# Performance work log

Hardware: AMD Instinct MI355X
Metric: run time of the kernel (lower is better)

The kernel has to match this reference:

```python
import jax, jax.numpy as jnp
import numpy as np


def setup_inputs() -> dict:
    key = jax.random.key(0)
    ks = jax.random.split(key, 8)
    B, L, D, H, Dh = 2, 2048, 1024, 16, 64
    scale = 1.0 / np.sqrt(D)
    return {
        "inputs_q": jax.random.normal(ks[0], (B, L, D), jnp.float32),
        "inputs_kv": jax.random.normal(ks[1], (B, L, D), jnp.float32),
        "mask_k": jax.random.uniform(ks[2], (B, L), jnp.float32),
        "Wq": jax.random.normal(ks[3], (D, H, Dh), jnp.float32) * scale,
        "bq": jnp.zeros((H, Dh), jnp.float32),
        "Wk": jax.random.normal(ks[4], (D, H, Dh), jnp.float32) * scale,
        "bk": jnp.zeros((H, Dh), jnp.float32),
        "Wv": jax.random.normal(ks[5], (D, H, Dh), jnp.float32) * scale,
        "bv": jnp.zeros((H, Dh), jnp.float32),
        "Wo": jax.random.normal(ks[6], (H, Dh, D), jnp.float32) * (1.0 / np.sqrt(D)),
        "bo": jnp.zeros((D,), jnp.float32),
    }


def reference(inputs_q, inputs_kv, mask_k, Wq, bq, Wk, bk, Wv, bv, Wo, bo):
    # QKV projections: [B,L,D] x [D,H,Dh] -> [B,L,H,Dh]
    q = jnp.einsum("bld,dhk->blhk", inputs_q, Wq) + bq
    k = jnp.einsum("bld,dhk->blhk", inputs_kv, Wk) + bk
    v = jnp.einsum("bld,dhk->blhk", inputs_kv, Wv) + bv
    # vector mask applied to values per key position
    v = mask_k[:, :, None, None] * v
    head_dim = q.shape[-1]
    q = q / jnp.sqrt(jnp.asarray(head_dim, q.dtype))
    # attention scores [B,H,Lq,Lk]
    scores = jnp.einsum("bqhk,bshk->bhqs", q, k)
    probs = jax.nn.softmax(scores, axis=-1)
    # weighted values [B,Lq,H,Dh]
    x = jnp.einsum("bhqs,bshk->bqhk", probs, v)
    # output projection over (head, head_dim)
    out = jnp.einsum("bqhk,hkd->bqd", x, Wo) + bo
    return out
```

## Files before the change

### kernel.cpp

```cpp
#include <hip/hip_runtime.h>
#include <stdint.h>

typedef __attribute__((ext_vector_type(8))) short bf16x8;
typedef __attribute__((ext_vector_type(4))) float f32x4;
typedef __attribute__((ext_vector_type(16))) float f32x16;
typedef __attribute__((ext_vector_type(4))) unsigned short us4;
typedef __attribute__((ext_vector_type(4))) unsigned int u32x4;

#define AS1 __attribute__((address_space(1)))
#define AS3 __attribute__((address_space(3)))

static constexpr int Lq = 2048;
static constexpr int Dm = 1024;
static constexpr int NH = 16;
static constexpr int DH = 64;

__device__ __forceinline__ unsigned short f2bf(float x) {
  union { float f; uint32_t u; } v; v.f = x;
  uint32_t r = v.u + 0x7FFFu + ((v.u >> 16) & 1u);
  return (unsigned short)(r >> 16);
}

#if __has_builtin(__builtin_amdgcn_exp2f)
__device__ __forceinline__ float exp2_fast(float x) { return __builtin_amdgcn_exp2f(x); }
#else
__device__ __forceinline__ float exp2_fast(float x) {
  float r; asm volatile("v_exp_f32 %0, %1" : "=v"(r) : "v"(x)); return r;
}
#endif

__device__ __forceinline__ uint32_t cvtpk_bf16(float lo, float hi) {
  uint32_t r;
  asm("v_cvt_pk_bf16_f32 %0, %1, %2" : "=v"(r) : "v"(lo), "v"(hi));
  return r;
}

__device__ __forceinline__ f32x16 zero16() {
  f32x16 z;
#pragma unroll
  for (int i = 0; i < 16; ++i) z[i] = 0.f;
  return z;
}

__global__ __launch_bounds__(256) void cvt2_kernel(
    const float* __restrict__ s0, const float* __restrict__ s1,
    unsigned short* __restrict__ d0, unsigned short* __restrict__ d1, int n4) {
  const float* src = blockIdx.y ? s1 : s0;
  unsigned short* dst = blockIdx.y ? d1 : d0;
  int idx = blockIdx.x * 256 + threadIdx.x;
  int stride = gridDim.x * 256;
  for (int i = idx; i < n4; i += stride) {
    float4 f = ((const float4*)src)[i];
    us4 o = { f2bf(f.x), f2bf(f.y), f2bf(f.z), f2bf(f.w) };
    ((us4*)dst)[i] = o;
  }
}

__global__ __launch_bounds__(256) void tpose_kernel(
    const float* __restrict__ W0, const float* __restrict__ W1,
    const float* __restrict__ W2, const float* __restrict__ W3,
    unsigned short* __restrict__ T0, unsigned short* __restrict__ T1,
    unsigned short* __restrict__ T2, unsigned short* __restrict__ T3) {
  __shared__ float tile[32][33];
  const float* src; unsigned short* dst;
  switch (blockIdx.z) {
    case 0: src = W0; dst = T0; break;
    case 1: src = W1; dst = T1; break;
    case 2: src = W2; dst = T2; break;
    default: src = W3; dst = T3; break;
  }
  int x = threadIdx.x & 31, ys = threadIdx.x >> 5;
  int bx = blockIdx.x * 32, by = blockIdx.y * 32;
  for (int i = 0; i < 4; ++i) {
    int y = ys * 4 + i;
    tile[y][x] = src[(size_t)(by + y) * Dm + bx + x];
  }
  __syncthreads();
  for (int i = 0; i < 4; ++i) {
    int y = ys * 4 + i;
    dst[(size_t)(bx + y) * Dm + by + x] = f2bf(tile[x][y]);
  }
}

__global__ __launch_bounds__(256) void gemm_kernel(
    const unsigned short* __restrict__ A0, const unsigned short* __restrict__ A1,
    const unsigned short* __restrict__ W0, const unsigned short* __restrict__ W1,
    const unsigned short* __restrict__ W2,
    const float* __restrict__ b0, const float* __restrict__ b1,
    const float* __restrict__ b2, const float* __restrict__ mask,
    unsigned short* __restrict__ Qw, unsigned short* __restrict__ Kw,
    unsigned short* __restrict__ Vtw, float* __restrict__ Of, int modeBase) {
  const int mode = modeBase + blockIdx.z;
  const unsigned short* Ap = (mode == 1 || mode == 2) ? A1 : A0;
  const unsigned short* Wp = (mode == 1) ? W1 : ((mode == 2) ? W2 : W0);
  const float* bias = (mode == 1) ? b1 : ((mode == 2) ? b2 : b0);

  const int tid = threadIdx.x, lane = tid & 63, wid = tid >> 6;
  const int wm = wid >> 1, wn = wid & 1;
  const int m0 = blockIdx.x * 128, n0 = blockIdx.y * 128;
  const int ln = lane & 15, kg = lane >> 4;

  __shared__ __align__(16) unsigned short smem[24576];

  f32x4 acc[4][4];
#pragma unroll
  for (int i = 0; i < 4; ++i)
#pragma unroll
    for (int j = 0; j < 4; ++j) acc[i][j] = f32x4{0.f, 0.f, 0.f, 0.f};

  auto stage_g = [&](int buf, int k0) {
#pragma unroll
    for (int i = 0; i < 2; ++i) {
      const int t = i * 256 + tid;
      const int row = t >> 2, ch = t & 3;
      const int tb = i * 256 + wid * 64;
      __builtin_amdgcn_global_load_lds(
          (const AS1 unsigned int*)(Ap + (size_t)(m0 + row) * Dm + k0 + ch * 8),
          (AS3 unsigned int*)&smem[buf * 4096 + tb * 8], 16, 0, 0);
      __builtin_amdgcn_global_load_lds(
          (const AS1 unsigned int*)(Wp + (size_t)(n0 + row) * Dm + k0 + ch * 8),
          (AS3 unsigned int*)&smem[12288 + buf * 4096 + tb * 8], 16, 0, 0);
    }
  };
  auto comp_g = [&](int buf) {
    const unsigned short* As = &smem[buf * 4096];
    const unsigned short* Bs = &smem[12288 + buf * 4096];
    bf16x8 af[4], bfv[4];
#pragma unroll
    for (int f = 0; f < 4; ++f) {
      af[f]  = *(const bf16x8*)&As[(wm * 64 + f * 16 + ln) * 32 + kg * 8];
      bfv[f] = *(const bf16x8*)&Bs[(wn * 64 + f * 16 + ln) * 32 + kg * 8];
    }
    __builtin_amdgcn_s_setprio(1);
#pragma unroll
    for (int mf = 0; mf < 4; ++mf)
#pragma unroll
      for (int nf = 0; nf < 4; ++nf)
        acc[mf][nf] = __builtin_amdgcn_mfma_f32_16x16x32_bf16(af[mf], bfv[nf],
                                                              acc[mf][nf], 0, 0, 0);
    __builtin_amdgcn_s_setprio(0);
  };

  stage_g(0, 0);
  stage_g(1, 32);
  for (int tt = 0; tt < 30; tt += 3) {
#pragma unroll
    for (int j = 0; j < 3; ++j) {
      const int t = tt + j;
      asm volatile("s_waitcnt vmcnt(4)" ::: "memory");
      asm volatile("s_barrier" ::: "memory");
      if (t < 30) stage_g((j + 2) % 3, (t + 2) * 32);
      comp_g(j);
    }
  }
  asm volatile("s_waitcnt vmcnt(4)" ::: "memory");
  asm volatile("s_barrier" ::: "memory");
  comp_g(0);
  asm volatile("s_waitcnt vmcnt(0)" ::: "memory");
  asm volatile("s_barrier" ::: "memory");
  comp_g(1);

  __syncthreads();
  unsigned short* ep = smem + wid * 2304;
  const int rowbase = m0 + wm * 64;
  const int colbase = n0 + wn * 64;

  if (mode <= 1) {
    unsigned short* dstbase = (mode == 0) ? Qw : Kw;
    const int hh = colbase >> 6;
    const int bb_ = rowbase >> 11, lb = rowbase & 2047;
    unsigned short* dst = dstbase + ((size_t)(bb_ * NH + hh) * Lq + lb) * DH;
    const float sc = (mode == 0) ? 0.18033688f : 1.0f;
    for (int p = 0; p < 2; ++p) {
      for (int nf = 0; nf < 4; ++nf) {
        const float bv_ = bias[colbase + nf * 16 + ln];
        for (int mh = 0; mh < 2; ++mh) {
          const int mf = 2 * p + mh;
          const int rl2 = mh * 16 + kg * 4;
          for (int r = 0; r < 4; ++r)
            ep[(rl2 + r) * 72 + nf * 16 + ln] = f2bf((acc[mf][nf][r] + bv_) * sc);
        }
      }
      for (int it = 0; it < 4; ++it) {
        const int e = it * 64 + lane;
        const int rr = e >> 3, c = (e & 7) * 8;
        *(bf16x8*)(dst + (size_t)(p * 32 + rr) * DH + c) = *(const bf16x8*)&ep[rr * 72 + c];
      }
    }
  } else if (mode == 2) {
    const int hh = colbase >> 6;
    const int bb_ = rowbase >> 11;
    const int l0 = rowbase & 2047;
    unsigned short* dst = Vtw + (size_t)(bb_ * NH + hh) * DH * Lq;
    for (int p = 0; p < 2; ++p) {
      for (int nh2 = 0; nh2 < 2; ++nh2) {
        const int nf = 2 * p + nh2;
        const int dh2 = nh2 * 16 + ln;
        const float bv_ = bias[colbase + nf * 16 + ln];
        for (int mf = 0; mf < 4; ++mf)
          for (int r = 0; r < 4; ++r) {
            const int rl = mf * 16 + kg * 4 + r;
            ep[dh2 * 72 + rl] = f2bf((acc[mf][nf][r] + bv_) * mask[rowbase + rl]);
          }
      }
      for (int it = 0; it < 4; ++it) {
        const int e = it * 64 + lane;
        const int dr = e >> 3, c = (e & 7) * 8;
        *(bf16x8*)(dst + (size_t)(p * 32 + dr) * Lq + l0 + c) = *(const bf16x8*)&ep[dr * 72 + c];
      }
    }
  } else {
    float* epf = (float*)smem + wid * 1152;
    for (int mf = 0; mf < 4; ++mf) {
      for (int nf = 0; nf < 4; ++nf) {
        const float bv_ = bias[colbase + nf * 16 + ln];
        for (int r = 0; r < 4; ++r)
          epf[(kg * 4 + r) * 68 + nf * 16 + ln] = acc[mf][nf][r] + bv_;
      }
      for (int it = 0; it < 4; ++it) {
        const int e = it * 64 + lane;
        const int rr = e >> 4, c = (lane & 15) * 4;
        *(f32x4*)(Of + (size_t)(rowbase + mf * 16 + rr) * Dm + colbase + c) =
            *(const f32x4*)&epf[rr * 68 + c];
      }
    }
  }
}

__global__ __launch_bounds__(512) void attn_kernel(
    const unsigned short* __restrict__ Q, const unsigned short* __restrict__ K,
    const unsigned short* __restrict__ Vt, unsigned short* __restrict__ X) {
  const int tid = threadIdx.x, lane = tid & 63, wv = tid >> 6;
  const int lq = lane & 31, hi = lane >> 5;
  const int wq = wv & 3, half = wv >> 2;
  const int h = blockIdx.y, b = blockIdx.z;
  const int q0 = blockIdx.x * 128 + wq * 32;

  const size_t bh = (size_t)b * NH + h;
  const unsigned short* Qp = Q + bh * Lq * DH;
  const unsigned short* Kp = K + bh * Lq * DH + (size_t)half * 1024 * DH;
  const unsigned short* Vp = Vt + bh * DH * Lq + half * 1024;

  __shared__ __align__(16) unsigned short smem[24576];
  unsigned short* Klds = smem + half * 12288;
  unsigned short* Vlds = smem + half * 12288 + 6144;

  const int st = tid & 255;
  const int kr = st >> 3, kc = st & 7;
  const unsigned short* ksrc = Kp + (size_t)kr * DH + ((kc ^ (kr & 7)) * 8);
  const int vr = st >> 2, vc = st & 3;
  const unsigned short* vsrc = Vp + (size_t)vr * Lq + ((vc ^ ((vr >> 1) & 3)) * 8);

  auto stage = [&](int buf, const unsigned short* kp, const unsigned short* vp) {
    __builtin_amdgcn_global_load_lds((const AS1 unsigned int*)kp,
        (AS3 unsigned int*)&Klds[buf * 2048 + wq * 512], 16, 0, 0);
    __builtin_amdgcn_global_load_lds((const AS1 unsigned int*)vp,
        (AS3 unsigned int*)&Vlds[buf * 2048 + wq * 512], 16, 0, 0);
  };

  bf16x8 qf[4];
#pragma unroll
  for (int ks = 0; ks < 4; ++ks)
    qf[ks] = *(const bf16x8*)(Qp + (size_t)(q0 + lq) * DH + ks * 16 + hi * 8);

  f32x16 o0 = zero16(), o1 = zero16();
  float lsum = 0.f;

  auto compute = [&](const unsigned short* Kb, const unsigned short* Vb) {
    f32x16 s0 = zero16(), s1 = zero16();
    __builtin_amdgcn_s_setprio(1);
#pragma unroll
    for (int ks = 0; ks < 4; ++ks) {
      const bf16x8 kfr =
          *(const bf16x8*)&Kb[lq * 64 + (((2 * ks + hi) ^ (lq & 7)) * 8)];
      if (ks < 2) s0 = __builtin_amdgcn_mfma_f32_32x32x16_bf16(kfr, qf[ks], s0, 0, 0, 0);
      else        s1 = __builtin_amdgcn_mfma_f32_32x32x16_bf16(kfr, qf[ks], s1, 0, 0, 0);
    }
    __builtin_amdgcn_s_setprio(0);

    float p[16];
#pragma unroll
    for (int i = 0; i < 16; ++i) p[i] = exp2_fast(s0[i] + s1[i]);
    lsum += ((((p[0] + p[1]) + (p[2] + p[3])) + ((p[4] + p[5]) + (p[6] + p[7]))) +
             (((p[8] + p[9]) + (p[10] + p[11])) + ((p[12] + p[13]) + (p[14] + p[15]))));

    uint32_t a00 = cvtpk_bf16(p[0],  p[1]),  a01 = cvtpk_bf16(p[2],  p[3]);
    uint32_t a10 = cvtpk_bf16(p[4],  p[5]),  a11 = cvtpk_bf16(p[6],  p[7]);
    uint32_t a20 = cvtpk_bf16(p[8],  p[9]),  a21 = cvtpk_bf16(p[10], p[11]);
    uint32_t a30 = cvtpk_bf16(p[12], p[13]), a31 = cvtpk_bf16(p[14], p[15]);
    asm volatile("v_permlane32_swap_b32 %0, %1" : "+v"(a00), "+v"(a10));
    asm volatile("v_permlane32_swap_b32 %0, %1" : "+v"(a01), "+v"(a11));
    asm volatile("v_permlane32_swap_b32 %0, %1" : "+v"(a20), "+v"(a30));
    asm volatile("v_permlane32_swap_b32 %0, %1" : "+v"(a21), "+v"(a31));
    u32x4 pw0 = {a00, a01, a10, a11};
    u32x4 pw1 = {a20, a21, a30, a31};
    const bf16x8 pa0 = *(const bf16x8*)&pw0;
    const bf16x8 pa1 = *(const bf16x8*)&pw1;

    __builtin_amdgcn_s_setprio(1);
    {
      const int sw0 = (lq >> 1) & 3;
      const bf16x8 vb0 = *(const bf16x8*)&Vb[lq * 32 + ((hi ^ sw0) * 8)];
      const bf16x8 vb1 = *(const bf16x8*)&Vb[lq * 32 + (((2 + hi) ^ sw0) * 8)];
      o0 = __builtin_amdgcn_mfma_f32_32x32x16_bf16(pa0, vb0, o0, 0, 0, 0);
      o0 = __builtin_amdgcn_mfma_f32_32x32x16_bf16(pa1, vb1, o0, 0, 0, 0);
      const int dh1 = 32 + lq;
      const int sw1 = (dh1 >> 1) & 3;
      const bf16x8 vb2 = *(const bf16x8*)&Vb[dh1 * 32 + ((hi ^ sw1) * 8)];
      const bf16x8 vb3 = *(const bf16x8*)&Vb[dh1 * 32 + (((2 + hi) ^ sw1) * 8)];
      o1 = __builtin_amdgcn_mfma_f32_32x32x16_bf16(pa0, vb2, o1, 0, 0, 0);
      o1 = __builtin_amdgcn_mfma_f32_32x32x16_bf16(pa1, vb3, o1, 0, 0, 0);
    }
    __builtin_amdgcn_s_setprio(0);
  };

  stage(0, ksrc, vsrc);
  stage(1, ksrc + 2048, vsrc + 32);
  const unsigned short* kpre = ksrc + 4096;
  const unsigned short* vpre = vsrc + 64;
  for (int tt = 0; tt < 30; tt += 3) {
#pragma unroll
    for (int j = 0; j < 3; ++j) {
      asm volatile("s_waitcnt vmcnt(2)" ::: "memory");
      asm volatile("s_barrier" ::: "memory");
      stage((j + 2) % 3, kpre, vpre);
      kpre += 2048; vpre += 32;
      compute(&Klds[j * 2048], &Vlds[j * 2048]);
    }
  }
  asm volatile("s_waitcnt vmcnt(2)" ::: "memory");
  asm volatile("s_barrier" ::: "memory");
  compute(&Klds[0], &Vlds[0]);
  asm volatile("s_waitcnt vmcnt(0)" ::: "memory");
  asm volatile("s_barrier" ::: "memory");
  compute(&Klds[2048], &Vlds[2048]);

  lsum += __shfl_xor(lsum, 32);
  __syncthreads();
  float* cs = (float*)smem;
  float* po = cs + wq * 2048;
  float* pl = cs + 8192 + wq * 32;
  if (half == 1) {
#pragma unroll
    for (int r = 0; r < 16; ++r) {
      const int qrow = (r & 3) + 8 * (r >> 2) + 4 * hi;
      po[qrow * 64 + lq]      = o0[r];
      po[qrow * 64 + 32 + lq] = o1[r];
    }
    if (hi == 0) pl[lq] = lsum;
  }
  __syncthreads();
  if (half == 0) {
#pragma unroll
    for (int r = 0; r < 16; ++r) {
      const int qrow = (r & 3) + 8 * (r >> 2) + 4 * hi;
      o0[r] += po[qrow * 64 + lq];
      o1[r] += po[qrow * 64 + 32 + lq];
    }
    lsum += pl[lq];
    const float inv = 1.0f / lsum;
    unsigned short* ep = (unsigned short*)po;
#pragma unroll
    for (int r = 0; r < 16; ++r) {
      const int qrow = (r & 3) + 8 * (r >> 2) + 4 * hi;
      const float iv = __shfl(inv, qrow);
      ep[qrow * 72 + lq]      = f2bf(o0[r] * iv);
      ep[qrow * 72 + 32 + lq] = f2bf(o1[r] * iv);
    }
#pragma unroll
    for (int it = 0; it < 4; ++it) {
      const int e = it * 64 + lane;
      const int row = e >> 3, ch = e & 7;
      *(bf16x8*)(X + (size_t)(b * Lq + q0 + row) * Dm + h * DH + ch * 8) =
          *(const bf16x8*)&ep[row * 72 + ch * 8];
    }
  }
}

extern "C" void kernel_launch(void* const* d_in, const int* in_sizes, int n_in,
                              void* d_out, int out_size, void* d_ws, size_t ws_size,
                              hipStream_t stream) {
  (void)in_sizes; (void)n_in; (void)out_size; (void)ws_size;
  const float* inputs_q  = (const float*)d_in[0];
  const float* inputs_kv = (const float*)d_in[1];
  const float* mask_k    = (const float*)d_in[2];
  const float* Wq = (const float*)d_in[3];
  const float* bq = (const float*)d_in[4];
  const float* Wk = (const float*)d_in[5];
  const float* bk = (const float*)d_in[6];
  const float* Wv = (const float*)d_in[7];
  const float* bv = (const float*)d_in[8];
  const float* Wo = (const float*)d_in[9];
  const float* bo = (const float*)d_in[10];
  float* out = (float*)d_out;

  unsigned short* ws = (unsigned short*)d_ws;
  const size_t BIG = 4194304;
  const size_t WSZ = 1048576;
  unsigned short* Xq  = ws;
  unsigned short* Xkv = Xq + BIG;
  unsigned short* Wqt = Xkv + BIG;
  unsigned short* Wkt = Wqt + WSZ;
  unsigned short* Wvt = Wkt + WSZ;
  unsigned short* Wot = Wvt + WSZ;
  unsigned short* Qw  = Wot + WSZ;
  unsigned short* Kw  = Qw + BIG;
  unsigned short* Vtw = Kw + BIG;
  unsigned short* Xat = Vtw + BIG;

  cvt2_kernel<<<dim3(512, 2), 256, 0, stream>>>(inputs_q, inputs_kv, Xq, Xkv,
                                                (int)(BIG / 4));
  tpose_kernel<<<dim3(32, 32, 4), 256, 0, stream>>>(Wq, Wk, Wv, Wo, Wqt, Wkt, Wvt, Wot);
  gemm_kernel<<<dim3(32, 8, 3), 256, 0, stream>>>(Xq, Xkv, Wqt, Wkt, Wvt, bq, bk, bv,
                                                  mask_k, Qw, Kw, Vtw, nullptr, 0);
  attn_kernel<<<dim3(16, 16, 2), 512, 0, stream>>>(Qw, Kw, Vtw, Xat);
  gemm_kernel<<<dim3(32, 8, 1), 256, 0, stream>>>(Xat, nullptr, Wot, nullptr, nullptr,
                                                  bo, nullptr, nullptr, nullptr,
                                                  nullptr, nullptr, nullptr, out, 3);
}
```

Before: 117.3 us.

## Use 8-wave GEMM blocks with swizzled LDS, MFMA row-sum in attention

The GEMM kernel now runs 512 threads per 128x128 tile, so each wave computes a 32x64 sub-tile, and LDS staging uses an XOR swizzle to cut bank conflicts on fragment reads. In attention, the two score accumulators are merged into one, and the softmax row sum is computed by an extra MFMA against a ones vector instead of scalar adds and a shuffle. The final normalisation is also restructured. This trades fewer accumulator registers per wave and more waves for less scalar work, at the cost of extra MFMA issue and bf16-rounded probabilities feeding the row sum.

```diff
diff --git a/kernel.cpp b/kernel.cpp
--- a/kernel.cpp
+++ b/kernel.cpp
@@ -82,7 +82,7 @@
   }
 }
 
-__global__ __launch_bounds__(256) void gemm_kernel(
+__global__ __launch_bounds__(512) void gemm_kernel(
     const unsigned short* __restrict__ A0, const unsigned short* __restrict__ A1,
     const unsigned short* __restrict__ W0, const unsigned short* __restrict__ W1,
     const unsigned short* __restrict__ W2,
@@ -102,38 +102,36 @@
 
   __shared__ __align__(16) unsigned short smem[24576];
 
-  f32x4 acc[4][4];
-#pragma unroll
-  for (int i = 0; i < 4; ++i)
+  f32x4 acc[2][4];
+#pragma unroll
+  for (int i = 0; i < 2; ++i)
 #pragma unroll
     for (int j = 0; j < 4; ++j) acc[i][j] = f32x4{0.f, 0.f, 0.f, 0.f};
 
+  const int srow = tid >> 2;
+  const int schx = (tid & 3) ^ ((srow >> 1) & 3);
   auto stage_g = [&](int buf, int k0) {
-#pragma unroll
-    for (int i = 0; i < 2; ++i) {
-      const int t = i * 256 + tid;
-      const int row = t >> 2, ch = t & 3;
-      const int tb = i * 256 + wid * 64;
-      __builtin_amdgcn_global_load_lds(
-          (const AS1 unsigned int*)(Ap + (size_t)(m0 + row) * Dm + k0 + ch * 8),
-          (AS3 unsigned int*)&smem[buf * 4096 + tb * 8], 16, 0, 0);
-      __builtin_amdgcn_global_load_lds(
-          (const AS1 unsigned int*)(Wp + (size_t)(n0 + row) * Dm + k0 + ch * 8),
-          (AS3 unsigned int*)&smem[12288 + buf * 4096 + tb * 8], 16, 0, 0);
-    }
+    __builtin_amdgcn_global_load_lds(
+        (const AS1 unsigned int*)(Ap + (size_t)(m0 + srow) * Dm + k0 + schx * 8),
+        (AS3 unsigned int*)&smem[buf * 4096 + wid * 512], 16, 0, 0);
+    __builtin_amdgcn_global_load_lds(
+        (const AS1 unsigned int*)(Wp + (size_t)(n0 + srow) * Dm + k0 + schx * 8),
+        (AS3 unsigned int*)&smem[12288 + buf * 4096 + wid * 512], 16, 0, 0);
   };
   auto comp_g = [&](int buf) {
     const unsigned short* As = &smem[buf * 4096];
     const unsigned short* Bs = &smem[12288 + buf * 4096];
-    bf16x8 af[4], bfv[4];
-#pragma unroll
-    for (int f = 0; f < 4; ++f) {
-      af[f]  = *(const bf16x8*)&As[(wm * 64 + f * 16 + ln) * 32 + kg * 8];
-      bfv[f] = *(const bf16x8*)&Bs[(wn * 64 + f * 16 + ln) * 32 + kg * 8];
-    }
+    const int rsw = kg ^ ((ln >> 1) & 3);
+    bf16x8 af[2], bfv[4];
+#pragma unroll
+    for (int f = 0; f < 2; ++f)
+      af[f] = *(const bf16x8*)&As[(wm * 32 + f * 16 + ln) * 32 + rsw * 8];
+#pragma unroll
+    for (int f = 0; f < 4; ++f)
+      bfv[f] = *(const bf16x8*)&Bs[(wn * 64 + f * 16 + ln) * 32 + rsw * 8];
     __builtin_amdgcn_s_setprio(1);
 #pragma unroll
-    for (int mf = 0; mf < 4; ++mf)
+    for (int mf = 0; mf < 2; ++mf)
 #pragma unroll
       for (int nf = 0; nf < 4; ++nf)
         acc[mf][nf] = __builtin_amdgcn_mfma_f32_16x16x32_bf16(af[mf], bfv[nf],
@@ -147,13 +145,13 @@
 #pragma unroll
     for (int j = 0; j < 3; ++j) {
       const int t = tt + j;
-      asm volatile("s_waitcnt vmcnt(4)" ::: "memory");
+      asm volatile("s_waitcnt vmcnt(2)" ::: "memory");
       asm volatile("s_barrier" ::: "memory");
       if (t < 30) stage_g((j + 2) % 3, (t + 2) * 32);
       comp_g(j);
     }
   }
-  asm volatile("s_waitcnt vmcnt(4)" ::: "memory");
+  asm volatile("s_waitcnt vmcnt(2)" ::: "memory");
   asm volatile("s_barrier" ::: "memory");
   comp_g(0);
   asm volatile("s_waitcnt vmcnt(0)" ::: "memory");
@@ -161,8 +159,8 @@
   comp_g(1);
 
   __syncthreads();
-  unsigned short* ep = smem + wid * 2304;
-  const int rowbase = m0 + wm * 64;
+  unsigned short* ep = smem + wid * 2560;
+  const int rowbase = m0 + wm * 32;
   const int colbase = n0 + wn * 64;
 
   if (mode <= 1) {
@@ -171,47 +169,40 @@
     const int bb_ = rowbase >> 11, lb = rowbase & 2047;
     unsigned short* dst = dstbase + ((size_t)(bb_ * NH + hh) * Lq + lb) * DH;
     const float sc = (mode == 0) ? 0.18033688f : 1.0f;
-    for (int p = 0; p < 2; ++p) {
-      for (int nf = 0; nf < 4; ++nf) {
-        const float bv_ = bias[colbase + nf * 16 + ln];
-        for (int mh = 0; mh < 2; ++mh) {
-          const int mf = 2 * p + mh;
-          const int rl2 = mh * 16 + kg * 4;
-          for (int r = 0; r < 4; ++r)
-            ep[(rl2 + r) * 72 + nf * 16 + ln] = f2bf((acc[mf][nf][r] + bv_) * sc);
-        }
-      }
-      for (int it = 0; it < 4; ++it) {
-        const int e = it * 64 + lane;
-        const int rr = e >> 3, c = (e & 7) * 8;
-        *(bf16x8*)(dst + (size_t)(p * 32 + rr) * DH + c) = *(const bf16x8*)&ep[rr * 72 + c];
-      }
+    for (int nf = 0; nf < 4; ++nf) {
+      const float bv_ = bias[colbase + nf * 16 + ln];
+      for (int mf = 0; mf < 2; ++mf)
+        for (int r = 0; r < 4; ++r)
+          ep[(mf * 16 + kg * 4 + r) * 72 + nf * 16 + ln] =
+              f2bf((acc[mf][nf][r] + bv_) * sc);
+    }
+    for (int it = 0; it < 4; ++it) {
+      const int e = it * 64 + lane;
+      const int rr = e >> 3, c = (e & 7) * 8;
+      *(bf16x8*)(dst + (size_t)rr * DH + c) = *(const bf16x8*)&ep[rr * 72 + c];
     }
   } else if (mode == 2) {
     const int hh = colbase >> 6;
     const int bb_ = rowbase >> 11;
     const int l0 = rowbase & 2047;
     unsigned short* dst = Vtw + (size_t)(bb_ * NH + hh) * DH * Lq;
-    for (int p = 0; p < 2; ++p) {
-      for (int nh2 = 0; nh2 < 2; ++nh2) {
-        const int nf = 2 * p + nh2;
-        const int dh2 = nh2 * 16 + ln;
-        const float bv_ = bias[colbase + nf * 16 + ln];
-        for (int mf = 0; mf < 4; ++mf)
-          for (int r = 0; r < 4; ++r) {
-            const int rl = mf * 16 + kg * 4 + r;
-            ep[dh2 * 72 + rl] = f2bf((acc[mf][nf][r] + bv_) * mask[rowbase + rl]);
-          }
-      }
-      for (int it = 0; it < 4; ++it) {
-        const int e = it * 64 + lane;
-        const int dr = e >> 3, c = (e & 7) * 8;
-        *(bf16x8*)(dst + (size_t)(p * 32 + dr) * Lq + l0 + c) = *(const bf16x8*)&ep[dr * 72 + c];
-      }
+    for (int nf = 0; nf < 4; ++nf) {
+      const int dh2 = nf * 16 + ln;
+      const float bv_ = bias[colbase + dh2];
+      for (int mf = 0; mf < 2; ++mf)
+        for (int r = 0; r < 4; ++r) {
+          const int rl = mf * 16 + kg * 4 + r;
+          ep[dh2 * 40 + rl] = f2bf((acc[mf][nf][r] + bv_) * mask[rowbase + rl]);
+        }
+    }
+    for (int it = 0; it < 4; ++it) {
+      const int e = it * 64 + lane;
+      const int dr = e >> 2, c = (e & 3) * 8;
+      *(bf16x8*)(dst + (size_t)dr * Lq + l0 + c) = *(const bf16x8*)&ep[dr * 40 + c];
     }
   } else {
-    float* epf = (float*)smem + wid * 1152;
-    for (int mf = 0; mf < 4; ++mf) {
+    float* epf = (float*)smem + wid * 1280;
+    for (int mf = 0; mf < 2; ++mf) {
       for (int nf = 0; nf < 4; ++nf) {
         const float bv_ = bias[colbase + nf * 16 + ln];
         for (int r = 0; r < 4; ++r)
@@ -263,26 +254,26 @@
   for (int ks = 0; ks < 4; ++ks)
     qf[ks] = *(const bf16x8*)(Qp + (size_t)(q0 + lq) * DH + ks * 16 + hi * 8);
 
-  f32x16 o0 = zero16(), o1 = zero16();
-  float lsum = 0.f;
+  bf16x8 onesf;
+#pragma unroll
+  for (int i = 0; i < 8; ++i) onesf[i] = (short)0x3F80;
+
+  f32x16 o0 = zero16(), o1 = zero16(), lacc = zero16();
 
   auto compute = [&](const unsigned short* Kb, const unsigned short* Vb) {
-    f32x16 s0 = zero16(), s1 = zero16();
+    f32x16 s = zero16();
     __builtin_amdgcn_s_setprio(1);
 #pragma unroll
     for (int ks = 0; ks < 4; ++ks) {
       const bf16x8 kfr =
           *(const bf16x8*)&Kb[lq * 64 + (((2 * ks + hi) ^ (lq & 7)) * 8)];
-      if (ks < 2) s0 = __builtin_amdgcn_mfma_f32_32x32x16_bf16(kfr, qf[ks], s0, 0, 0, 0);
-      else        s1 = __builtin_amdgcn_mfma_f32_32x32x16_bf16(kfr, qf[ks], s1, 0, 0, 0);
+      s = __builtin_amdgcn_mfma_f32_32x32x16_bf16(kfr, qf[ks], s, 0, 0, 0);
     }
     __builtin_amdgcn_s_setprio(0);
 
     float p[16];
 #pragma unroll
-    for (int i = 0; i < 16; ++i) p[i] = exp2_fast(s0[i] + s1[i]);
-    lsum += ((((p[0] + p[1]) + (p[2] + p[3])) + ((p[4] + p[5]) + (p[6] + p[7]))) +
-             (((p[8] + p[9]) + (p[10] + p[11])) + ((p[12] + p[13]) + (p[14] + p[15]))));
+    for (int i = 0; i < 16; ++i) p[i] = exp2_fast(s[i]);
 
     uint32_t a00 = cvtpk_bf16(p[0],  p[1]),  a01 = cvtpk_bf16(p[2],  p[3]);
     uint32_t a10 = cvtpk_bf16(p[4],  p[5]),  a11 = cvtpk_bf16(p[6],  p[7]);
@@ -298,6 +289,8 @@
     const bf16x8 pa1 = *(const bf16x8*)&pw1;
 
     __builtin_amdgcn_s_setprio(1);
+    lacc = __builtin_amdgcn_mfma_f32_32x32x16_bf16(pa0, onesf, lacc, 0, 0, 0);
+    lacc = __builtin_amdgcn_mfma_f32_32x32x16_bf16(pa1, onesf, lacc, 0, 0, 0);
     {
       const int sw0 = (lq >> 1) & 3;
       const bf16x8 vb0 = *(const bf16x8*)&Vb[lq * 32 + ((hi ^ sw0) * 8)];
@@ -335,7 +328,6 @@
   asm volatile("s_barrier" ::: "memory");
   compute(&Klds[2048], &Vlds[2048]);
 
-  lsum += __shfl_xor(lsum, 32);
   __syncthreads();
   float* cs = (float*)smem;
   float* po = cs + wq * 2048;
@@ -347,25 +339,28 @@
       po[qrow * 64 + lq]      = o0[r];
       po[qrow * 64 + 32 + lq] = o1[r];
     }
-    if (hi == 0) pl[lq] = lsum;
+    if (lq == 0) {
+#pragma unroll
+      for (int r = 0; r < 16; ++r)
+        pl[(r & 3) + 8 * (r >> 2) + 4 * hi] = lacc[r];
+    }
   }
   __syncthreads();
   if (half == 0) {
+    unsigned short ou0[16], ou1[16];
 #pragma unroll
     for (int r = 0; r < 16; ++r) {
       const int qrow = (r & 3) + 8 * (r >> 2) + 4 * hi;
-      o0[r] += po[qrow * 64 + lq];
-      o1[r] += po[qrow * 64 + 32 + lq];
-    }
-    lsum += pl[lq];
-    const float inv = 1.0f / lsum;
+      const float iv = 1.0f / (lacc[r] + pl[qrow]);
+      ou0[r] = f2bf((o0[r] + po[qrow * 64 + lq]) * iv);
+      ou1[r] = f2bf((o1[r] + po[qrow * 64 + 32 + lq]) * iv);
+    }
     unsigned short* ep = (unsigned short*)po;
 #pragma unroll
     for (int r = 0; r < 16; ++r) {
       const int qrow = (r & 3) + 8 * (r >> 2) + 4 * hi;
-      const float iv = __shfl(inv, qrow);
-      ep[qrow * 72 + lq]      = f2bf(o0[r] * iv);
-      ep[qrow * 72 + 32 + lq] = f2bf(o1[r] * iv);
+      ep[qrow * 72 + lq]      = ou0[r];
+      ep[qrow * 72 + 32 + lq] = ou1[r];
     }
 #pragma unroll
     for (int it = 0; it < 4; ++it) {
@@ -411,10 +406,10 @@
   cvt2_kernel<<<dim3(512, 2), 256, 0, stream>>>(inputs_q, inputs_kv, Xq, Xkv,
                                                 (int)(BIG / 4));
   tpose_kernel<<<dim3(32, 32, 4), 256, 0, stream>>>(Wq, Wk, Wv, Wo, Wqt, Wkt, Wvt, Wot);
-  gemm_kernel<<<dim3(32, 8, 3), 256, 0, stream>>>(Xq, Xkv, Wqt, Wkt, Wvt, bq, bk, bv,
+  gemm_kernel<<<dim3(32, 8, 3), 512, 0, stream>>>(Xq, Xkv, Wqt, Wkt, Wvt, bq, bk, bv,
                                                   mask_k, Qw, Kw, Vtw, nullptr, 0);
   attn_kernel<<<dim3(16, 16, 2), 512, 0, stream>>>(Qw, Kw, Vtw, Xat);
-  gemm_kernel<<<dim3(32, 8, 1), 256, 0, stream>>>(Xat, nullptr, Wot, nullptr, nullptr,
+  gemm_kernel<<<dim3(32, 8, 1), 512, 0, stream>>>(Xat, nullptr, Wot, nullptr, nullptr,
                                                   bo, nullptr, nullptr, nullptr,
                                                   nullptr, nullptr, nullptr, out, 3);
 }
```

New measurement: 104.6 us. 1.12x faster.
